# Kernel tuning notes

Hardware: AMD Instinct MI355X
Metric: run time of the kernel (lower is better)

Reference implementation:

```python
import jax, jax.numpy as jnp
import numpy as np

B, C_IN, C_OUT, N, K = 16, 128, 128, 4096, 16


def setup_inputs() -> dict:
    key = jax.random.key(0)
    k1, k2, k3, k4 = jax.random.split(key, 4)
    x = jax.random.normal(k1, (B, C_IN, N, 1), dtype=jnp.float32)
    edge_index = jax.random.randint(k2, (2, B, N, K), 0, N, dtype=jnp.int32)
    # 1x1 conv weight of BasicConv([C_IN, C_OUT], 'relu', None, bias=False)
    W = jax.random.normal(k3, (C_OUT, C_IN), dtype=jnp.float32) * (1.0 / np.sqrt(C_IN))
    # module bias param, initialized to zeros; use random here to exercise the add
    bias = jax.random.normal(k4, (1, C_OUT, 1, 1), dtype=jnp.float32) * 0.01
    return {"x": x, "edge_index": edge_index, "W": W, "bias": bias}


def reference(x, edge_index, W, bias):
    b, _, n, _ = x.shape
    # BasicConv: 1x1 conv (no bias) + ReLU
    h = jax.nn.relu(jnp.einsum('oi,binu->bonu', W, x))  # [B, C_out, N, 1]
    h2 = h[..., 0]                                       # [B, C_out, N]
    # add_self_loops: append self index along neighbor dim
    self_idx = jnp.broadcast_to(jnp.arange(n, dtype=edge_index.dtype)[None, None, :, None],
                                (2, b, n, 1))
    ei = jnp.concatenate([edge_index, self_idx], axis=-1)  # [2, B, N, K+1]
    idx = ei[0]                                            # [B, N, K+1]
    deg = ei.shape[-1]
    norm = 1.0 / deg
    # batched_index_select: gather neighbor features -> [B, C_out, N, K+1]
    x_j = jax.vmap(lambda hb, ib: hb[:, ib])(h2, idx)
    aggr = (x_j * norm).sum(axis=-1, keepdims=True)        # [B, C_out, N, 1]
    return aggr + bias
```

## Files before the change

### kernel.cpp

```cpp
#include <hip/hip_runtime.h>

#define B_    16
#define CIN_  128
#define COUT_ 128
#define N_    4096
#define K_    16

typedef __attribute__((ext_vector_type(8))) short bf16x8;
typedef __attribute__((ext_vector_type(4))) float f32x4;
typedef __attribute__((ext_vector_type(4))) int   i32x4;

__device__ inline unsigned short f2bf(float f) {
  unsigned u = __float_as_uint(f);
  u += 0x7fffu + ((u >> 16) & 1u);
  return (unsigned short)(u >> 16);
}

__global__ __launch_bounds__(256) void convW_k(
    const float* __restrict__ W, unsigned short* __restrict__ Wbf) {
  int id = blockIdx.x * 256 + threadIdx.x;
  float4 v = reinterpret_cast<const float4*>(W)[id];
  unsigned p0 = (unsigned)f2bf(v.x) | ((unsigned)f2bf(v.y) << 16);
  unsigned p1 = (unsigned)f2bf(v.z) | ((unsigned)f2bf(v.w) << 16);
  *reinterpret_cast<uint2*>(Wbf + 4 * id) = make_uint2(p0, p1);
}

__global__ __launch_bounds__(256) void gemm_relu_k(
    const unsigned short* __restrict__ Wbf, const float* __restrict__ x,
    unsigned short* __restrict__ h) {
  __shared__ unsigned short Wl[128 * 136];
  const int tid = threadIdx.x;
  const int l   = blockIdx.x;
  const int b   = ((l & 7) << 1) | ((l >> 3) >> 6);
  const int n0  = ((l >> 3) & 63) * 64;

#pragma unroll
  for (int r = 0; r < 8; ++r) {
    int id  = tid + 256 * r;
    int co  = id >> 4;
    int seg = id & 15;
    uint4 v = reinterpret_cast<const uint4*>(Wbf)[id];
    *reinterpret_cast<uint4*>(&Wl[co * 136 + 8 * seg]) = v;
  }
  __syncthreads();

  const int lane = tid & 63;
  const int w    = tid >> 6;
  const int m    = lane & 15;
  const int quad = lane >> 4;

  const float* xb = x + (size_t)b * CIN_ * N_ + n0 + 16 * w + m;
  bf16x8 a[4];
#pragma unroll
  for (int s = 0; s < 4; ++s) {
#pragma unroll
    for (int j = 0; j < 8; ++j) {
      int ci = 32 * s + 8 * quad + j;
      a[s][j] = (short)f2bf(xb[(size_t)ci * N_]);
    }
  }

  const int rbase = n0 + 16 * w + 4 * quad;
  unsigned short* hb = h + (size_t)b * N_ * COUT_;
#pragma unroll
  for (int t = 0; t < 8; ++t) {
    f32x4 c = {0.f, 0.f, 0.f, 0.f};
#pragma unroll
    for (int s = 0; s < 4; ++s) {
      bf16x8 bf = *reinterpret_cast<const bf16x8*>(
          &Wl[(16 * t + m) * 136 + 32 * s + 8 * quad]);
      c = __builtin_amdgcn_mfma_f32_16x16x32_bf16(a[s], bf, c, 0, 0, 0);
    }
    int co = 16 * t + m;
#pragma unroll
    for (int r = 0; r < 4; ++r) {
      float v = c[r] > 0.f ? c[r] : 0.f;
      hb[(size_t)(rbase + r) * COUT_ + co] = f2bf(v);
    }
  }
}

__global__ __launch_bounds__(256, 4) void aggr_k(
    const unsigned short* __restrict__ h, const int* __restrict__ ei,
    const float* __restrict__ bias, float* __restrict__ out) {
  __shared__ int idx_t[17 * 64];
  const int tid  = threadIdx.x;
  const int l    = blockIdx.x;
  const int rest = l >> 3;
  const int b    = ((l & 7) << 1) | (rest >> 6);
  const int n0   = (rest & 63) * 64;

  {
    int n  = tid >> 2;
    int kq = tid & 3;
    i32x4 v = __builtin_nontemporal_load(
        reinterpret_cast<const i32x4*>(ei + ((size_t)b * N_ + n0 + n) * K_) + kq);
    idx_t[(4 * kq + 0) * 64 + n] = v.x;
    idx_t[(4 * kq + 1) * 64 + n] = v.y;
    idx_t[(4 * kq + 2) * 64 + n] = v.z;
    idx_t[(4 * kq + 3) * 64 + n] = v.w;
    if (tid < 64) idx_t[16 * 64 + tid] = n0 + tid;
  }
  __syncthreads();

  const int q = tid & 15;
  const int g = tid >> 4;
  const unsigned short* hb = h + (size_t)b * N_ * COUT_;

  float acc[4][8];
#pragma unroll
  for (int j = 0; j < 4; ++j)
#pragma unroll
    for (int c = 0; c < 8; ++c) acc[j][c] = 0.f;

#pragma unroll 2
  for (int k = 0; k < 17; ++k) {
    uint4 v[4];
#pragma unroll
    for (int j = 0; j < 4; ++j) {
      int node = idx_t[k * 64 + 4 * g + j];
      v[j] = *reinterpret_cast<const uint4*>(hb + (size_t)node * COUT_ + 8 * q);
    }
#pragma unroll
    for (int j = 0; j < 4; ++j) {
      acc[j][0] += __uint_as_float(v[j].x << 16);
      acc[j][1] += __uint_as_float(v[j].x & 0xffff0000u);
      acc[j][2] += __uint_as_float(v[j].y << 16);
      acc[j][3] += __uint_as_float(v[j].y & 0xffff0000u);
      acc[j][4] += __uint_as_float(v[j].z << 16);
      acc[j][5] += __uint_as_float(v[j].z & 0xffff0000u);
      acc[j][6] += __uint_as_float(v[j].w << 16);
      acc[j][7] += __uint_as_float(v[j].w & 0xffff0000u);
    }
  }

  const float norm = 1.0f / 17.0f;
  const float4 bv0 = *reinterpret_cast<const float4*>(bias + 8 * q);
  const float4 bv1 = *reinterpret_cast<const float4*>(bias + 8 * q + 4);
  float* ob = out + (size_t)b * COUT_ * N_ + n0 + 4 * g;
#pragma unroll
  for (int c = 0; c < 8; ++c) {
    int co = 8 * q + c;
    float bb = (c < 4) ? ((c == 0) ? bv0.x : (c == 1) ? bv0.y : (c == 2) ? bv0.z : bv0.w)
                       : ((c == 4) ? bv1.x : (c == 5) ? bv1.y : (c == 6) ? bv1.z : bv1.w);
    float4 r;
    r.x = acc[0][c] * norm + bb;
    r.y = acc[1][c] * norm + bb;
    r.z = acc[2][c] * norm + bb;
    r.w = acc[3][c] * norm + bb;
    *reinterpret_cast<float4*>(ob + (size_t)co * N_) = r;
  }
}

extern "C" void kernel_launch(void* const* d_in, const int* in_sizes, int n_in,
                              void* d_out, int out_size, void* d_ws, size_t ws_size,
                              hipStream_t stream) {
  const float* x    = (const float*)d_in[0];
  const int*   ei   = (const int*)d_in[1];
  const float* W    = (const float*)d_in[2];
  const float* bias = (const float*)d_in[3];
  float* out = (float*)d_out;
  unsigned short* h   = (unsigned short*)d_ws;
  unsigned short* Wbf = (unsigned short*)((char*)d_ws + (size_t)B_ * N_ * COUT_ * 2);

  convW_k<<<dim3(16), 256, 0, stream>>>(W, Wbf);
  gemm_relu_k<<<dim3(B_ * N_ / 64), 256, 0, stream>>>(Wbf, x, h);
  aggr_k<<<dim3(B_ * N_ / 64), 256, 0, stream>>>(h, ei, bias, out);
}
```

Measured before the change: 116.9 us.

## Stage GEMM output in LDS for coalesced stores, enlarge blocks to 1024 threads

```diff
diff --git a/kernel.cpp b/kernel.cpp
--- a/kernel.cpp
+++ b/kernel.cpp
@@ -25,18 +25,20 @@
   *reinterpret_cast<uint2*>(Wbf + 4 * id) = make_uint2(p0, p1);
 }
 
-__global__ __launch_bounds__(256) void gemm_relu_k(
+__global__ __launch_bounds__(1024, 4) void gemm_relu_k(
     const unsigned short* __restrict__ Wbf, const float* __restrict__ x,
     unsigned short* __restrict__ h) {
   __shared__ unsigned short Wl[128 * 136];
-  const int tid = threadIdx.x;
-  const int l   = blockIdx.x;
-  const int b   = ((l & 7) << 1) | ((l >> 3) >> 6);
-  const int n0  = ((l >> 3) & 63) * 64;
+  __shared__ unsigned short He[256 * 144];
+  const int tid  = threadIdx.x;
+  const int l    = blockIdx.x;
+  const int slot = l >> 3;
+  const int b    = ((l & 7) << 1) | (slot >> 4);
+  const int n0   = (slot & 15) * 256;
 
 #pragma unroll
-  for (int r = 0; r < 8; ++r) {
-    int id  = tid + 256 * r;
+  for (int r = 0; r < 2; ++r) {
+    int id  = tid + 1024 * r;
     int co  = id >> 4;
     int seg = id & 15;
     uint4 v = reinterpret_cast<const uint4*>(Wbf)[id];
@@ -52,16 +54,12 @@
   const float* xb = x + (size_t)b * CIN_ * N_ + n0 + 16 * w + m;
   bf16x8 a[4];
 #pragma unroll
-  for (int s = 0; s < 4; ++s) {
+  for (int s = 0; s < 4; ++s)
 #pragma unroll
-    for (int j = 0; j < 8; ++j) {
-      int ci = 32 * s + 8 * quad + j;
-      a[s][j] = (short)f2bf(xb[(size_t)ci * N_]);
-    }
-  }
+    for (int j = 0; j < 8; ++j)
+      a[s][j] = (short)f2bf(xb[(size_t)(32 * s + 8 * quad + j) * N_]);
 
-  const int rbase = n0 + 16 * w + 4 * quad;
-  unsigned short* hb = h + (size_t)b * N_ * COUT_;
+  const int nrow = 16 * w + 4 * quad;
 #pragma unroll
   for (int t = 0; t < 8; ++t) {
     f32x4 c = {0.f, 0.f, 0.f, 0.f};
@@ -75,8 +73,19 @@
 #pragma unroll
     for (int r = 0; r < 4; ++r) {
       float v = c[r] > 0.f ? c[r] : 0.f;
-      hb[(size_t)(rbase + r) * COUT_ + co] = f2bf(v);
+      He[(nrow + r) * 144 + co] = f2bf(v);
     }
+  }
+  __syncthreads();
+
+  unsigned short* hb = h + ((size_t)b * N_ + n0) * COUT_;
+  const int seg = tid & 15;
+  const int nr  = tid >> 4;
+#pragma unroll
+  for (int p = 0; p < 4; ++p) {
+    int n = nr + 64 * p;
+    uint4 v = *reinterpret_cast<const uint4*>(&He[n * 144 + 8 * seg]);
+    *reinterpret_cast<uint4*>(hb + (size_t)n * COUT_ + 8 * seg) = v;
   }
 }
 
@@ -164,6 +173,6 @@
   unsigned short* Wbf = (unsigned short*)((char*)d_ws + (size_t)B_ * N_ * COUT_ * 2);
 
   convW_k<<<dim3(16), 256, 0, stream>>>(W, Wbf);
-  gemm_relu_k<<<dim3(B_ * N_ / 64), 256, 0, stream>>>(Wbf, x, h);
+  gemm_relu_k<<<dim3(256), 1024, 0, stream>>>(Wbf, x, h);
   aggr_k<<<dim3(B_ * N_ / 64), 256, 0, stream>>>(h, ei, bias, out);
 }
```

Result: faster. 112.5 us (-3.8%).
